# Optimization experiments

Measured on AMD Instinct MI355X. Metric: run time of the kernel, lower is better.

## Reference

```python
import jax, jax.numpy as jnp
import numpy as np

H, KVH, D, BS, L = 32, 8, 128, 16, 4096
MAX_BLOCKS = L // BS          # 256 blocks per sequence (sink cache capacity)
B = 16
NUM_BLOCKS = B * MAX_BLOCKS   # 4096 total cache blocks
T = MAX_BLOCKS * BS           # 4096 linearized cache slots per sequence
SCALE = 1.0 / np.sqrt(D)


def _rope_cos_sin(pos):
    # neox-style RoPE tables; pos: int array [...]. returns cos/sin [..., D/2]
    inv_freq = 1.0 / (10000.0 ** (jnp.arange(0, D, 2, dtype=jnp.float32) / D))
    ang = pos[..., None].astype(jnp.float32) * inv_freq
    return jnp.cos(ang), jnp.sin(ang)


def _apply_rope(x, cos, sin):
    # x [..., D]; cos/sin broadcastable to x[..., :D//2]
    x1, x2 = jnp.split(x, 2, axis=-1)
    return jnp.concatenate([x1 * cos - x2 * sin, x2 * cos + x1 * sin], axis=-1)


def setup_inputs() -> dict:
    key = jax.random.key(0)
    ks = jax.random.split(key, 6)
    q = jax.random.normal(ks[0], (B, H * D), dtype=jnp.float32)
    k = jax.random.normal(ks[1], (B, KVH * D), dtype=jnp.float32)
    v = jax.random.normal(ks[2], (B, KVH * D), dtype=jnp.float32)
    key_cache = jax.random.normal(ks[3], (NUM_BLOCKS, BS, KVH, D), dtype=jnp.float32)
    value_cache = jax.random.normal(ks[4], (NUM_BLOCKS, BS, KVH, D), dtype=jnp.float32)
    block_tables = jnp.arange(B * MAX_BLOCKS, dtype=jnp.int32).reshape(B, MAX_BLOCKS)
    context_lens = jax.random.randint(ks[5], (B,), 0, 6000, dtype=jnp.int32)
    return {"q": q, "k": k, "v": v, "key_cache": key_cache,
            "value_cache": value_cache, "block_tables": block_tables,
            "context_lens": context_lens}


def reference(q, k, v, key_cache, value_cache, block_tables, context_lens):
    ctx = context_lens.astype(jnp.int32)                         # [B] past tokens
    rem = ctx % BS
    # sink/rolling cap: if past >= model_context_len, effective seq len caps
    seq_len = jnp.where(ctx >= L, L - BS + rem + 1, ctx + 1)     # [B]
    pos_q = seq_len - 1                                          # capped current position

    # gather pre-rope keys/values from paged cache -> [B, T, KVH, D]
    keys = key_cache[block_tables].reshape(B, T, KVH, D)
    vals = value_cache[block_tables].reshape(B, T, KVH, D)

    # re-apply rope to gathered keys at their cache-relative positions 0..T-1
    cos_k, sin_k = _rope_cos_sin(jnp.arange(T))                  # [T, D/2]
    keys = _apply_rope(keys, cos_k[None, :, None, :], sin_k[None, :, None, :])

    # rope current q, k at capped positions
    cos_q, sin_q = _rope_cos_sin(pos_q)                          # [B, D/2]
    qh = _apply_rope(q.reshape(B, H, D), cos_q[:, None, :], sin_q[:, None, :])
    kh = _apply_rope(k.reshape(B, KVH, D), cos_q[:, None, :], sin_q[:, None, :])

    # scatter current token's k/v at its slot (offset rem in last used block == seq_len-1)
    bidx = jnp.arange(B)
    keys = keys.at[bidx, pos_q].set(kh)
    vals = vals.at[bidx, pos_q].set(v.reshape(B, KVH, D))

    # GQA attention over first seq_len cached tokens
    G = H // KVH
    qg = qh.reshape(B, KVH, G, D)
    scores = jnp.einsum('bhgd,bthd->bhgt', qg, keys) * SCALE     # [B, KVH, G, T]
    mask = jnp.arange(T)[None, :] < seq_len[:, None]             # [B, T]
    scores = jnp.where(mask[:, None, None, :], scores, jnp.finfo(scores.dtype).min)
    probs = jax.nn.softmax(scores, axis=-1)
    out = jnp.einsum('bhgt,bthd->bhgd', probs, vals)             # [B, KVH, G, D]
    return out.reshape(B, H * D)
```

## Files before the change

### kernel.cpp

```cpp
#include <hip/hip_runtime.h>
#include <math.h>

#define B_      16
#define H_      32
#define KVH_    8
#define G_      4
#define D_      128
#define BS_     16
#define L_      4096
#define MAXB_   256
#define T_      4096
#define NPART_  16
#define PART_   256
#define SCALE_  0.08838834764831843f

__device__ __forceinline__ int seq_len_of(int ctx) {
  return (ctx >= L_) ? (L_ - BS_ + (ctx & (BS_ - 1)) + 1) : (ctx + 1);
}

__global__ void rope_table_kernel(float* __restrict__ tab) {
  int idx = blockIdx.x * blockDim.x + threadIdx.x;
  if (idx >= T_ * 64) return;
  int t = idx >> 6, i = idx & 63;
  double inv = pow(10000.0, -(double)(2 * i) / 128.0);
  float ang = (float)t * (float)inv;
  double a = (double)ang;
  tab[2 * idx]     = (float)cos(a);
  tab[2 * idx + 1] = (float)sin(a);
}


#define LOADK(P, tt)                                                        \
  {                                                                         \
    int tcl_  = min((tt), t1m1);                                            \
    int blk_  = sblk[(tcl_ - t0) >> 4];                                     \
    int base_ = ((blk_ * BS_ + (tcl_ & (BS_ - 1))) * KVH_ + kvh) * D_;      \
    const float4* kc4_ = (const float4*)(kc + base_);                       \
    const float4* vc4_ = (const float4*)(vc + base_);                       \
    P##ka = kc4_[dg];      P##kb = kc4_[16 + dg];                           \
    P##va = vc4_[dg];      P##vb = vc4_[16 + dg];                           \
  }

#define COMPUTE(P, tt)                                                      \
  {                                                                         \
    float kr1[4], kr2[4];                                                   \
    kr1[0] = P##ka.x * cc0.x - P##kb.x * cc0.y;                             \
    kr2[0] = P##kb.x * cc0.x + P##ka.x * cc0.y;                             \
    kr1[1] = P##ka.y * cc0.z - P##kb.y * cc0.w;                             \
    kr2[1] = P##kb.y * cc0.z + P##ka.y * cc0.w;                             \
    kr1[2] = P##ka.z * cc1.x - P##kb.z * cc1.y;                             \
    kr2[2] = P##kb.z * cc1.x + P##ka.z * cc1.y;                             \
    kr1[3] = P##ka.w * cc1.z - P##kb.w * cc1.w;                             \
    kr2[3] = P##kb.w * cc1.z + P##ka.w * cc1.w;                             \
    bool valid_ = ((tt) < t1) & ((tt) != posq);                             \
    float s[G_];                                                            \
    _Pragma("unroll")                                                       \
    for (int g = 0; g < G_; ++g) {                                          \
      s[g] = kr1[0] * q1[g][0] + kr2[0] * q2[g][0]                          \
           + kr1[1] * q1[g][1] + kr2[1] * q2[g][1]                          \
           + kr1[2] * q1[g][2] + kr2[2] * q2[g][2]                          \
           + kr1[3] * q1[g][3] + kr2[3] * q2[g][3];                         \
    }                                                                       \
    _Pragma("unroll")                                                       \
    for (int off = 1; off <= 8; off <<= 1) {                                \
      _Pragma("unroll")                                                     \
      for (int g = 0; g < G_; ++g) s[g] += __shfl_xor(s[g], off);           \
    }                                                                       \
    _Pragma("unroll")                                                       \
    for (int g = 0; g < G_; ++g) {                                          \
      float sv   = valid_ ? s[g] : -1e30f;                                  \
      float mn   = fmaxf(m[g], sv);                                         \
      float corr = __expf(m[g] - mn);                                       \
      float p    = __expf(sv - mn);                                         \
      p = valid_ ? p : 0.0f;                                                \
      m[g] = mn;                                                            \
      l[g] = l[g] * corr + p;                                               \
      acc[g][0] = acc[g][0] * corr + p * P##va.x;                           \
      acc[g][1] = acc[g][1] * corr + p * P##va.y;                           \
      acc[g][2] = acc[g][2] * corr + p * P##va.z;                           \
      acc[g][3] = acc[g][3] * corr + p * P##va.w;                           \
      acc[g][4] = acc[g][4] * corr + p * P##vb.x;                           \
      acc[g][5] = acc[g][5] * corr + p * P##vb.y;                           \
      acc[g][6] = acc[g][6] * corr + p * P##vb.z;                           \
      acc[g][7] = acc[g][7] * corr + p * P##vb.w;                           \
    }                                                                       \
    {                     \
      float nc_;                                                            \
      nc_ = cc0.x * r0.x - cc0.y * r0.y;                                    \
      cc0.y = cc0.y * r0.x + cc0.x * r0.y; cc0.x = nc_;                     \
      nc_ = cc0.z * r0.z - cc0.w * r0.w;                                    \
      cc0.w = cc0.w * r0.z + cc0.z * r0.w; cc0.z = nc_;                     \
      nc_ = cc1.x * r1.x - cc1.y * r1.y;                                    \
      cc1.y = cc1.y * r1.x + cc1.x * r1.y; cc1.x = nc_;                     \
      nc_ = cc1.z * r1.z - cc1.w * r1.w;                                    \
      cc1.w = cc1.w * r1.z + cc1.z * r1.w; cc1.z = nc_;                     \
    }                                                                       \
  }

__global__ __launch_bounds__(256) void attn_partial_kernel(
    const float* __restrict__ q, const float* __restrict__ knew,
    const float* __restrict__ vnew, const float* __restrict__ kc,
    const float* __restrict__ vc, const int* __restrict__ btab,
    const int* __restrict__ ctxl, const float* __restrict__ tab,
    float* __restrict__ opart, float2* __restrict__ ml) {
  int bid  = blockIdx.x;
  int part = bid & (NPART_ - 1);
  int kvh  = (bid >> 4) & (KVH_ - 1);
  int b    = bid >> 7;

  int seq = seq_len_of(ctxl[b]);
  int t0 = part * PART_;
  if (t0 >= seq) return;
  int t1 = min(t0 + PART_, seq);
  int t1m1 = t1 - 1;
  int posq = seq - 1;

  int lane = threadIdx.x & 63;
  int wave = threadIdx.x >> 6;
  int tsub = lane >> 4;
  int dg   = lane & 15;

  __shared__ int sblk[PART_ / BS_];
  if (threadIdx.x < PART_ / BS_)
    sblk[threadIdx.x] = btab[b * MAXB_ + (t0 >> 4) + threadIdx.x];
  __syncthreads();

  const float4* tab4 = (const float4*)tab;

  int tstart = t0 + 4 * wave + tsub;
  float4 cc0 = tab4[tstart * 32 + 2 * dg];
  float4 cc1 = tab4[tstart * 32 + 2 * dg + 1];
  float4 r0  = tab4[16 * 32 + 2 * dg];
  float4 r1  = tab4[16 * 32 + 2 * dg + 1];

  float q1[G_][4], q2[G_][4];
  {
    float4 cq0 = tab4[posq * 32 + 2 * dg];
    float4 cq1 = tab4[posq * 32 + 2 * dg + 1];
#pragma unroll
    for (int g = 0; g < G_; ++g) {
      const float* qp = q + b * (H_ * D_) + (kvh * G_ + g) * D_;
      float4 a  = *(const float4*)(qp + 4 * dg);
      float4 bq = *(const float4*)(qp + 64 + 4 * dg);
      q1[g][0] = (a.x * cq0.x - bq.x * cq0.y) * SCALE_;
      q2[g][0] = (bq.x * cq0.x + a.x * cq0.y) * SCALE_;
      q1[g][1] = (a.y * cq0.z - bq.y * cq0.w) * SCALE_;
      q2[g][1] = (bq.y * cq0.z + a.y * cq0.w) * SCALE_;
      q1[g][2] = (a.z * cq1.x - bq.z * cq1.y) * SCALE_;
      q2[g][2] = (bq.z * cq1.x + a.z * cq1.y) * SCALE_;
      q1[g][3] = (a.w * cq1.z - bq.w * cq1.w) * SCALE_;
      q2[g][3] = (bq.w * cq1.z + a.w * cq1.w) * SCALE_;
    }
  }

  float m[G_], l[G_], acc[G_][8];
#pragma unroll
  for (int g = 0; g < G_; ++g) {
    m[g] = -1e30f; l[g] = 0.f;
#pragma unroll
    for (int j = 0; j < 8; ++j) acc[g][j] = 0.f;
  }

  {
    float4 Aka, Akb, Ava, Avb;
    float4 Bka, Bkb, Bva, Bvb;
    float4 Cka, Ckb, Cva, Cvb;
    float4 Dka, Dkb, Dva, Dvb;
    int nIter = ((t1 - t0 + 15) >> 4);
    nIter = (nIter + 3) & ~3;
    int t = tstart;
    LOADK(A, t);
    LOADK(B, t + 16);
    for (int it = 0; it < nIter; it += 4) {
      LOADK(C, t + 32);  COMPUTE(A, t);  t += 16;
      LOADK(D, t + 32);  COMPUTE(B, t);  t += 16;
      LOADK(A, t + 32);  COMPUTE(C, t);  t += 16;
      LOADK(B, t + 32);  COMPUTE(D, t);  t += 16;
    }
  }

  if (threadIdx.x < 16 && posq >= t0 && posq < t1) {
    const float* kp = knew + (b * KVH_ + kvh) * D_;
    float4 xa = *(const float4*)(kp + 4 * dg);
    float4 xb = *(const float4*)(kp + 64 + 4 * dg);
    float4 p0 = tab4[posq * 32 + 2 * dg];
    float4 p1 = tab4[posq * 32 + 2 * dg + 1];
    float kr1[4], kr2[4];
    kr1[0] = xa.x * p0.x - xb.x * p0.y;  kr2[0] = xb.x * p0.x + xa.x * p0.y;
    kr1[1] = xa.y * p0.z - xb.y * p0.w;  kr2[1] = xb.y * p0.z + xa.y * p0.w;
    kr1[2] = xa.z * p1.x - xb.z * p1.y;  kr2[2] = xb.z * p1.x + xa.z * p1.y;
    kr1[3] = xa.w * p1.z - xb.w * p1.w;  kr2[3] = xb.w * p1.z + xa.w * p1.w;
    const float* vp = vnew + (b * KVH_ + kvh) * D_;
    float4 va_ = *(const float4*)(vp + 4 * dg);
    float4 vb_ = *(const float4*)(vp + 64 + 4 * dg);
    float s[G_];
#pragma unroll
    for (int g = 0; g < G_; ++g) {
      s[g] = kr1[0] * q1[g][0] + kr2[0] * q2[g][0]
           + kr1[1] * q1[g][1] + kr2[1] * q2[g][1]
           + kr1[2] * q1[g][2] + kr2[2] * q2[g][2]
           + kr1[3] * q1[g][3] + kr2[3] * q2[g][3];
    }
#pragma unroll
    for (int off = 1; off <= 8; off <<= 1) {
#pragma unroll
      for (int g = 0; g < G_; ++g) s[g] += __shfl_xor(s[g], off);
    }
#pragma unroll
    for (int g = 0; g < G_; ++g) {
      float sv   = s[g];
      float mn   = fmaxf(m[g], sv);
      float corr = __expf(m[g] - mn);
      float p    = __expf(sv - mn);
      m[g] = mn;
      l[g] = l[g] * corr + p;
      acc[g][0] = acc[g][0] * corr + p * va_.x;
      acc[g][1] = acc[g][1] * corr + p * va_.y;
      acc[g][2] = acc[g][2] * corr + p * va_.z;
      acc[g][3] = acc[g][3] * corr + p * va_.w;
      acc[g][4] = acc[g][4] * corr + p * vb_.x;
      acc[g][5] = acc[g][5] * corr + p * vb_.y;
      acc[g][6] = acc[g][6] * corr + p * vb_.z;
      acc[g][7] = acc[g][7] * corr + p * vb_.w;
    }
  }

  auto merge_off = [&](int off) {
#pragma unroll
    for (int g = 0; g < G_; ++g) {
      float mo = __shfl_xor(m[g], off);
      float lo = __shfl_xor(l[g], off);
      float M  = fmaxf(m[g], mo);
      float fa = __expf(m[g] - M);
      float fb = __expf(mo - M);
      l[g] = l[g] * fa + lo * fb;
      m[g] = M;
#pragma unroll
      for (int j = 0; j < 8; ++j) {
        float ao = __shfl_xor(acc[g][j], off);
        acc[g][j] = acc[g][j] * fa + ao * fb;
      }
    }
  };
  merge_off(16);
  merge_off(32);

  __shared__ float  lds_acc[4][G_][D_];
  __shared__ float2 lds_ml[4][G_];
  if (lane < 16) {
#pragma unroll
    for (int g = 0; g < G_; ++g) {
#pragma unroll
      for (int j = 0; j < 8; ++j) {
        int dim = (j < 4) ? (4 * dg + j) : (64 + 4 * dg + (j - 4));
        lds_acc[wave][g][dim] = acc[g][j];
      }
      if (lane == 0) lds_ml[wave][g] = make_float2(m[g], l[g]);
    }
  }
  __syncthreads();
  if (wave == 0) {
    int w = tsub;
#pragma unroll
    for (int g = 0; g < G_; ++g) {
      float2 t2 = lds_ml[w][g];
      m[g] = t2.x; l[g] = t2.y;
#pragma unroll
      for (int j = 0; j < 8; ++j) {
        int dim = (j < 4) ? (4 * dg + j) : (64 + 4 * dg + (j - 4));
        acc[g][j] = lds_acc[w][g][dim];
      }
    }
    merge_off(16);
    merge_off(32);
    if (lane < 16) {
#pragma unroll
      for (int g = 0; g < G_; ++g) {
        float* op = opart + (size_t)(bid * G_ + g) * D_;
#pragma unroll
        for (int j = 0; j < 8; ++j) {
          int dim = (j < 4) ? (4 * dg + j) : (64 + 4 * dg + (j - 4));
          op[dim] = acc[g][j];
        }
        if (lane == 0) ml[bid * G_ + g] = make_float2(m[g], l[g]);
      }
    }
  }
}

__global__ void attn_reduce_kernel(const float* __restrict__ opart,
                                   const float2* __restrict__ ml,
                                   const int* __restrict__ ctxl,
                                   float* __restrict__ out) {
  int bh = blockIdx.x;
  int b = bh >> 5, h = bh & 31;
  int kvh = h >> 2, g = h & 3;
  int d = threadIdx.x;
  int seq = seq_len_of(ctxl[b]);
  int nlive = (seq + PART_ - 1) / PART_;
  int base = (b * KVH_ + kvh) * NPART_;

  float M = -1e30f;
  for (int p = 0; p < nlive; ++p) M = fmaxf(M, ml[(base + p) * G_ + g].x);
  float L = 0.f, O = 0.f;
  for (int p = 0; p < nlive; ++p) {
    float2 mlv = ml[(base + p) * G_ + g];
    float f = __expf(mlv.x - M);
    L += mlv.y * f;
    O += opart[(size_t)((base + p) * G_ + g) * D_ + d] * f;
  }
  out[b * (H_ * D_) + h * D_ + d] = O / L;
}

extern "C" void kernel_launch(void* const* d_in, const int* in_sizes, int n_in,
                              void* d_out, int out_size, void* d_ws, size_t ws_size,
                              hipStream_t stream) {
  const float* q    = (const float*)d_in[0];
  const float* k    = (const float*)d_in[1];
  const float* v    = (const float*)d_in[2];
  const float* kc   = (const float*)d_in[3];
  const float* vc   = (const float*)d_in[4];
  const int*   btab = (const int*)d_in[5];
  const int*   ctxl = (const int*)d_in[6];
  float* out = (float*)d_out;

  float*  tab   = (float*)d_ws;
  float*  opart = tab + (size_t)T_ * 64 * 2;
  float2* ml    = (float2*)(opart + (size_t)B_ * KVH_ * NPART_ * G_ * D_);

  rope_table_kernel<<<(T_ * 64 + 255) / 256, 256, 0, stream>>>(tab);
  attn_partial_kernel<<<B_ * KVH_ * NPART_, 256, 0, stream>>>(
      q, k, v, kc, vc, btab, ctxl, tab, opart, ml);
  attn_reduce_kernel<<<B_ * H_, D_, 0, stream>>>(opart, ml, ctxl, out);
}
```

Measured before the change: 125.3 us.

## Split attention into single-wave blocks with 64-token partitions

Each attention partition shrinks from 256 to 64 tokens, and each block becomes a single 64-thread wave, with four times as many partitions. This removes the LDS cross-wave merge and both __syncthreads, and block-table indices are loaded as one int4 packed into a 64-bit register instead of going through shared memory. Partial outputs are written with float4 stores. In exchange the software pipeline is only two stages deep, and the reduce kernel must combine up to 64 partials per head, which adds workspace traffic.

```diff
diff --git a/kernel.cpp b/kernel.cpp
--- a/kernel.cpp
+++ b/kernel.cpp
@@ -10,9 +10,11 @@
 #define L_      4096
 #define MAXB_   256
 #define T_      4096
-#define NPART_  16
-#define PART_   256
+#define NPART_  64
+#define PART_   64
 #define SCALE_  0.08838834764831843f
+
+typedef unsigned long long ull;
 
 __device__ __forceinline__ int seq_len_of(int ctx) {
   return (ctx >= L_) ? (L_ - BS_ + (ctx & (BS_ - 1)) + 1) : (ctx + 1);
@@ -33,7 +35,7 @@
 #define LOADK(P, tt)                                                        \
   {                                                                         \
     int tcl_  = min((tt), t1m1);                                            \
-    int blk_  = sblk[(tcl_ - t0) >> 4];                                     \
+    int blk_  = (int)((packed >> (((tcl_ - t0) >> 4) * 16)) & 0xFFFF);      \
     int base_ = ((blk_ * BS_ + (tcl_ & (BS_ - 1))) * KVH_ + kvh) * D_;      \
     const float4* kc4_ = (const float4*)(kc + base_);                       \
     const float4* vc4_ = (const float4*)(vc + base_);                       \
@@ -84,7 +86,7 @@
       acc[g][6] = acc[g][6] * corr + p * P##vb.z;                           \
       acc[g][7] = acc[g][7] * corr + p * P##vb.w;                           \
     }                                                                       \
-    {                     \
+    {                      \
       float nc_;                                                            \
       nc_ = cc0.x * r0.x - cc0.y * r0.y;                                    \
       cc0.y = cc0.y * r0.x + cc0.x * r0.y; cc0.x = nc_;                     \
@@ -97,7 +99,7 @@
     }                                                                       \
   }
 
-__global__ __launch_bounds__(256) void attn_partial_kernel(
+__global__ __launch_bounds__(64, 4) void attn_partial_kernel(
     const float* __restrict__ q, const float* __restrict__ knew,
     const float* __restrict__ vnew, const float* __restrict__ kc,
     const float* __restrict__ vc, const int* __restrict__ btab,
@@ -105,8 +107,8 @@
     float* __restrict__ opart, float2* __restrict__ ml) {
   int bid  = blockIdx.x;
   int part = bid & (NPART_ - 1);
-  int kvh  = (bid >> 4) & (KVH_ - 1);
-  int b    = bid >> 7;
+  int kvh  = (bid >> 6) & (KVH_ - 1);
+  int b    = bid >> 9;
 
   int seq = seq_len_of(ctxl[b]);
   int t0 = part * PART_;
@@ -115,23 +117,21 @@
   int t1m1 = t1 - 1;
   int posq = seq - 1;
 
-  int lane = threadIdx.x & 63;
-  int wave = threadIdx.x >> 6;
+  int lane = threadIdx.x;
   int tsub = lane >> 4;
   int dg   = lane & 15;
 
-  __shared__ int sblk[PART_ / BS_];
-  if (threadIdx.x < PART_ / BS_)
-    sblk[threadIdx.x] = btab[b * MAXB_ + (t0 >> 4) + threadIdx.x];
-  __syncthreads();
+  int4 bi = *(const int4*)(btab + b * MAXB_ + (t0 >> 4));
+  ull packed = (ull)(unsigned)bi.x | ((ull)(unsigned)bi.y << 16)
+             | ((ull)(unsigned)bi.z << 32) | ((ull)(unsigned)bi.w << 48);
 
   const float4* tab4 = (const float4*)tab;
 
-  int tstart = t0 + 4 * wave + tsub;
+  int tstart = t0 + tsub;
   float4 cc0 = tab4[tstart * 32 + 2 * dg];
   float4 cc1 = tab4[tstart * 32 + 2 * dg + 1];
-  float4 r0  = tab4[16 * 32 + 2 * dg];
-  float4 r1  = tab4[16 * 32 + 2 * dg + 1];
+  float4 r0  = tab4[4 * 32 + 2 * dg];
+  float4 r1  = tab4[4 * 32 + 2 * dg + 1];
 
   float q1[G_][4], q2[G_][4];
   {
@@ -164,22 +164,17 @@
   {
     float4 Aka, Akb, Ava, Avb;
     float4 Bka, Bkb, Bva, Bvb;
-    float4 Cka, Ckb, Cva, Cvb;
-    float4 Dka, Dkb, Dva, Dvb;
-    int nIter = ((t1 - t0 + 15) >> 4);
-    nIter = (nIter + 3) & ~3;
+    int nIter = (t1 - t0 + 3) >> 2;
+    nIter = (nIter + 1) & ~1;
     int t = tstart;
     LOADK(A, t);
-    LOADK(B, t + 16);
-    for (int it = 0; it < nIter; it += 4) {
-      LOADK(C, t + 32);  COMPUTE(A, t);  t += 16;
-      LOADK(D, t + 32);  COMPUTE(B, t);  t += 16;
-      LOADK(A, t + 32);  COMPUTE(C, t);  t += 16;
-      LOADK(B, t + 32);  COMPUTE(D, t);  t += 16;
-    }
-  }
-
-  if (threadIdx.x < 16 && posq >= t0 && posq < t1) {
+    for (int it = 0; it < nIter; it += 2) {
+      LOADK(B, t + 4);  COMPUTE(A, t);  t += 4;
+      LOADK(A, t + 4);  COMPUTE(B, t);  t += 4;
+    }
+  }
+
+  if (lane < 16 && posq >= t0 && posq < t1) {
     const float* kp = knew + (b * KVH_ + kvh) * D_;
     float4 xa = *(const float4*)(kp + 4 * dg);
     float4 xb = *(const float4*)(kp + 64 + 4 * dg);
@@ -225,7 +220,8 @@
     }
   }
 
-  auto merge_off = [&](int off) {
+#pragma unroll
+  for (int off = 16; off <= 32; off <<= 1) {
 #pragma unroll
     for (int g = 0; g < G_; ++g) {
       float mo = __shfl_xor(m[g], off);
@@ -241,49 +237,15 @@
         acc[g][j] = acc[g][j] * fa + ao * fb;
       }
     }
-  };
-  merge_off(16);
-  merge_off(32);
-
-  __shared__ float  lds_acc[4][G_][D_];
-  __shared__ float2 lds_ml[4][G_];
+  }
+
   if (lane < 16) {
 #pragma unroll
     for (int g = 0; g < G_; ++g) {
-#pragma unroll
-      for (int j = 0; j < 8; ++j) {
-        int dim = (j < 4) ? (4 * dg + j) : (64 + 4 * dg + (j - 4));
-        lds_acc[wave][g][dim] = acc[g][j];
-      }
-      if (lane == 0) lds_ml[wave][g] = make_float2(m[g], l[g]);
-    }
-  }
-  __syncthreads();
-  if (wave == 0) {
-    int w = tsub;
-#pragma unroll
-    for (int g = 0; g < G_; ++g) {
-      float2 t2 = lds_ml[w][g];
-      m[g] = t2.x; l[g] = t2.y;
-#pragma unroll
-      for (int j = 0; j < 8; ++j) {
-        int dim = (j < 4) ? (4 * dg + j) : (64 + 4 * dg + (j - 4));
-        acc[g][j] = lds_acc[w][g][dim];
-      }
-    }
-    merge_off(16);
-    merge_off(32);
-    if (lane < 16) {
-#pragma unroll
-      for (int g = 0; g < G_; ++g) {
-        float* op = opart + (size_t)(bid * G_ + g) * D_;
-#pragma unroll
-        for (int j = 0; j < 8; ++j) {
-          int dim = (j < 4) ? (4 * dg + j) : (64 + 4 * dg + (j - 4));
-          op[dim] = acc[g][j];
-        }
-        if (lane == 0) ml[bid * G_ + g] = make_float2(m[g], l[g]);
-      }
+      float* op = opart + (size_t)(bid * G_ + g) * D_;
+      *(float4*)(op + 4 * dg)      = make_float4(acc[g][0], acc[g][1], acc[g][2], acc[g][3]);
+      *(float4*)(op + 64 + 4 * dg) = make_float4(acc[g][4], acc[g][5], acc[g][6], acc[g][7]);
+      if (lane == 0) ml[bid * G_ + g] = make_float2(m[g], l[g]);
     }
   }
 }
@@ -329,7 +291,7 @@
   float2* ml    = (float2*)(opart + (size_t)B_ * KVH_ * NPART_ * G_ * D_);
 
   rope_table_kernel<<<(T_ * 64 + 255) / 256, 256, 0, stream>>>(tab);
-  attn_partial_kernel<<<B_ * KVH_ * NPART_, 256, 0, stream>>>(
+  attn_partial_kernel<<<B_ * KVH_ * NPART_, 64, 0, stream>>>(
       q, k, v, kc, vc, btab, ctxl, tab, opart, ml);
   attn_reduce_kernel<<<B_ * H_, D_, 0, stream>>>(opart, ml, ctxl, out);
 }
```

Result: slower. 196.5 us (+56.9%).

## Compute RoPE cos/sin inline and drop table kernel; tighten loop bounds

Applied to the files above, without the earlier changes.

Removes the separate RoPE table kernel and its 2 MB workspace table. Each thread now computes its starting, step and query cos/sin values in-kernel with double-precision sincos. The KV loop changes from a 4-deep, padded-to-multiple-of-4 pipeline with clamped loads to a 2-deep ping-pong that stops exactly at the partition end. This removes wasted masked iterations and one kernel launch. In exchange, each thread pays for double-precision transcendentals up front and has less load prefetch depth.

```diff
diff --git a/kernel.cpp b/kernel.cpp
--- a/kernel.cpp
+++ b/kernel.cpp
@@ -18,23 +18,11 @@
   return (ctx >= L_) ? (L_ - BS_ + (ctx & (BS_ - 1)) + 1) : (ctx + 1);
 }
 
-__global__ void rope_table_kernel(float* __restrict__ tab) {
-  int idx = blockIdx.x * blockDim.x + threadIdx.x;
-  if (idx >= T_ * 64) return;
-  int t = idx >> 6, i = idx & 63;
-  double inv = pow(10000.0, -(double)(2 * i) / 128.0);
-  float ang = (float)t * (float)inv;
-  double a = (double)ang;
-  tab[2 * idx]     = (float)cos(a);
-  tab[2 * idx + 1] = (float)sin(a);
-}
-
 
 #define LOADK(P, tt)                                                        \
   {                                                                         \
-    int tcl_  = min((tt), t1m1);                                            \
-    int blk_  = sblk[(tcl_ - t0) >> 4];                                     \
-    int base_ = ((blk_ * BS_ + (tcl_ & (BS_ - 1))) * KVH_ + kvh) * D_;      \
+    int blk_  = sblk[((tt) - t0) >> 4];                                     \
+    int base_ = ((blk_ * BS_ + ((tt) & (BS_ - 1))) * KVH_ + kvh) * D_;      \
     const float4* kc4_ = (const float4*)(kc + base_);                       \
     const float4* vc4_ = (const float4*)(vc + base_);                       \
     P##ka = kc4_[dg];      P##kb = kc4_[16 + dg];                           \
@@ -52,7 +40,7 @@
     kr2[2] = P##kb.z * cc1.x + P##ka.z * cc1.y;                             \
     kr1[3] = P##ka.w * cc1.z - P##kb.w * cc1.w;                             \
     kr2[3] = P##kb.w * cc1.z + P##ka.w * cc1.w;                             \
-    bool valid_ = ((tt) < t1) & ((tt) != posq);                             \
+    bool valid_ = ((tt) != posq);                                           \
     float s[G_];                                                            \
     _Pragma("unroll")                                                       \
     for (int g = 0; g < G_; ++g) {                                          \
@@ -101,7 +89,7 @@
     const float* __restrict__ q, const float* __restrict__ knew,
     const float* __restrict__ vnew, const float* __restrict__ kc,
     const float* __restrict__ vc, const int* __restrict__ btab,
-    const int* __restrict__ ctxl, const float* __restrict__ tab,
+    const int* __restrict__ ctxl,
     float* __restrict__ opart, float2* __restrict__ ml) {
   int bid  = blockIdx.x;
   int part = bid & (NPART_ - 1);
@@ -112,7 +100,6 @@
   int t0 = part * PART_;
   if (t0 >= seq) return;
   int t1 = min(t0 + PART_, seq);
-  int t1m1 = t1 - 1;
   int posq = seq - 1;
 
   int lane = threadIdx.x & 63;
@@ -125,32 +112,46 @@
     sblk[threadIdx.x] = btab[b * MAXB_ + (t0 >> 4) + threadIdx.x];
   __syncthreads();
 
-  const float4* tab4 = (const float4*)tab;
-
   int tstart = t0 + 4 * wave + tsub;
-  float4 cc0 = tab4[tstart * 32 + 2 * dg];
-  float4 cc1 = tab4[tstart * 32 + 2 * dg + 1];
-  float4 r0  = tab4[16 * 32 + 2 * dg];
-  float4 r1  = tab4[16 * 32 + 2 * dg + 1];
+  float4 cc0, cc1, r0, r1, cq0, cq1;
+  {
+    float ft = (float)tstart, fq = (float)posq;
+    float cs[3][8];
+#pragma unroll
+    for (int j = 0; j < 4; ++j) {
+      double invd = pow(10000.0, -(double)(8 * dg + 2 * j) / 128.0);
+      float invf = (float)invd;
+      float angs[3] = {ft * invf, 16.0f * invf, fq * invf};
+#pragma unroll
+      for (int u = 0; u < 3; ++u) {
+        double sn, csn;
+        sincos((double)angs[u], &sn, &csn);
+        cs[u][2 * j]     = (float)csn;
+        cs[u][2 * j + 1] = (float)sn;
+      }
+    }
+    cc0 = make_float4(cs[0][0], cs[0][1], cs[0][2], cs[0][3]);
+    cc1 = make_float4(cs[0][4], cs[0][5], cs[0][6], cs[0][7]);
+    r0  = make_float4(cs[1][0], cs[1][1], cs[1][2], cs[1][3]);
+    r1  = make_float4(cs[1][4], cs[1][5], cs[1][6], cs[1][7]);
+    cq0 = make_float4(cs[2][0], cs[2][1], cs[2][2], cs[2][3]);
+    cq1 = make_float4(cs[2][4], cs[2][5], cs[2][6], cs[2][7]);
+  }
 
   float q1[G_][4], q2[G_][4];
-  {
-    float4 cq0 = tab4[posq * 32 + 2 * dg];
-    float4 cq1 = tab4[posq * 32 + 2 * dg + 1];
-#pragma unroll
-    for (int g = 0; g < G_; ++g) {
-      const float* qp = q + b * (H_ * D_) + (kvh * G_ + g) * D_;
-      float4 a  = *(const float4*)(qp + 4 * dg);
-      float4 bq = *(const float4*)(qp + 64 + 4 * dg);
-      q1[g][0] = (a.x * cq0.x - bq.x * cq0.y) * SCALE_;
-      q2[g][0] = (bq.x * cq0.x + a.x * cq0.y) * SCALE_;
-      q1[g][1] = (a.y * cq0.z - bq.y * cq0.w) * SCALE_;
-      q2[g][1] = (bq.y * cq0.z + a.y * cq0.w) * SCALE_;
-      q1[g][2] = (a.z * cq1.x - bq.z * cq1.y) * SCALE_;
-      q2[g][2] = (bq.z * cq1.x + a.z * cq1.y) * SCALE_;
-      q1[g][3] = (a.w * cq1.z - bq.w * cq1.w) * SCALE_;
-      q2[g][3] = (bq.w * cq1.z + a.w * cq1.w) * SCALE_;
-    }
+#pragma unroll
+  for (int g = 0; g < G_; ++g) {
+    const float* qp = q + b * (H_ * D_) + (kvh * G_ + g) * D_;
+    float4 a  = *(const float4*)(qp + 4 * dg);
+    float4 bq = *(const float4*)(qp + 64 + 4 * dg);
+    q1[g][0] = (a.x * cq0.x - bq.x * cq0.y) * SCALE_;
+    q2[g][0] = (bq.x * cq0.x + a.x * cq0.y) * SCALE_;
+    q1[g][1] = (a.y * cq0.z - bq.y * cq0.w) * SCALE_;
+    q2[g][1] = (bq.y * cq0.z + a.y * cq0.w) * SCALE_;
+    q1[g][2] = (a.z * cq1.x - bq.z * cq1.y) * SCALE_;
+    q2[g][2] = (bq.z * cq1.x + a.z * cq1.y) * SCALE_;
+    q1[g][3] = (a.w * cq1.z - bq.w * cq1.w) * SCALE_;
+    q2[g][3] = (bq.w * cq1.z + a.w * cq1.w) * SCALE_;
   }
 
   float m[G_], l[G_], acc[G_][8];
@@ -164,18 +165,21 @@
   {
     float4 Aka, Akb, Ava, Avb;
     float4 Bka, Bkb, Bva, Bvb;
-    float4 Cka, Ckb, Cva, Cvb;
-    float4 Dka, Dkb, Dva, Dvb;
-    int nIter = ((t1 - t0 + 15) >> 4);
-    nIter = (nIter + 3) & ~3;
     int t = tstart;
-    LOADK(A, t);
-    LOADK(B, t + 16);
-    for (int it = 0; it < nIter; it += 4) {
-      LOADK(C, t + 32);  COMPUTE(A, t);  t += 16;
-      LOADK(D, t + 32);  COMPUTE(B, t);  t += 16;
-      LOADK(A, t + 32);  COMPUTE(C, t);  t += 16;
-      LOADK(B, t + 32);  COMPUTE(D, t);  t += 16;
+    if (t < t1) {
+      LOADK(A, t);
+      while (1) {
+        int t2 = t + 16;
+        if (t2 < t1) LOADK(B, t2);
+        COMPUTE(A, t);
+        t = t2;
+        if (t >= t1) break;
+        t2 = t + 16;
+        if (t2 < t1) LOADK(A, t2);
+        COMPUTE(B, t);
+        t = t2;
+        if (t >= t1) break;
+      }
     }
   }
 
@@ -183,13 +187,11 @@
     const float* kp = knew + (b * KVH_ + kvh) * D_;
     float4 xa = *(const float4*)(kp + 4 * dg);
     float4 xb = *(const float4*)(kp + 64 + 4 * dg);
-    float4 p0 = tab4[posq * 32 + 2 * dg];
-    float4 p1 = tab4[posq * 32 + 2 * dg + 1];
     float kr1[4], kr2[4];
-    kr1[0] = xa.x * p0.x - xb.x * p0.y;  kr2[0] = xb.x * p0.x + xa.x * p0.y;
-    kr1[1] = xa.y * p0.z - xb.y * p0.w;  kr2[1] = xb.y * p0.z + xa.y * p0.w;
-    kr1[2] = xa.z * p1.x - xb.z * p1.y;  kr2[2] = xb.z * p1.x + xa.z * p1.y;
-    kr1[3] = xa.w * p1.z - xb.w * p1.w;  kr2[3] = xb.w * p1.z + xa.w * p1.w;
+    kr1[0] = xa.x * cq0.x - xb.x * cq0.y;  kr2[0] = xb.x * cq0.x + xa.x * cq0.y;
+    kr1[1] = xa.y * cq0.z - xb.y * cq0.w;  kr2[1] = xb.y * cq0.z + xa.y * cq0.w;
+    kr1[2] = xa.z * cq1.x - xb.z * cq1.y;  kr2[2] = xb.z * cq1.x + xa.z * cq1.y;
+    kr1[3] = xa.w * cq1.z - xb.w * cq1.w;  kr2[3] = xb.w * cq1.z + xa.w * cq1.w;
     const float* vp = vnew + (b * KVH_ + kvh) * D_;
     float4 va_ = *(const float4*)(vp + 4 * dg);
     float4 vb_ = *(const float4*)(vp + 64 + 4 * dg);
@@ -276,7 +278,7 @@
     if (lane < 16) {
 #pragma unroll
       for (int g = 0; g < G_; ++g) {
-        float* op = opart + (size_t)(bid * G_ + g) * D_;
+        float* op = opart + (size_t)((bid)*G_ + g) * D_;
 #pragma unroll
         for (int j = 0; j < 8; ++j) {
           int dim = (j < 4) ? (4 * dg + j) : (64 + 4 * dg + (j - 4));
@@ -324,12 +326,10 @@
   const int*   ctxl = (const int*)d_in[6];
   float* out = (float*)d_out;
 
-  float*  tab   = (float*)d_ws;
-  float*  opart = tab + (size_t)T_ * 64 * 2;
+  float*  opart = (float*)d_ws;
   float2* ml    = (float2*)(opart + (size_t)B_ * KVH_ * NPART_ * G_ * D_);
 
-  rope_table_kernel<<<(T_ * 64 + 255) / 256, 256, 0, stream>>>(tab);
   attn_partial_kernel<<<B_ * KVH_ * NPART_, 256, 0, stream>>>(
-      q, k, v, kc, vc, btab, ctxl, tab, opart, ml);
+      q, k, v, kc, vc, btab, ctxl, opart, ml);
   attn_reduce_kernel<<<B_ * H_, D_, 0, stream>>>(opart, ml, ctxl, out);
 }
```

Measured after the change: 119.2 us. -4.8%, faster.
